# Kernel tuning notes

Hardware: AMD Instinct MI355X
Metric: run time of the kernel (lower is better)

## Reference

```python
import jax, jax.numpy as jnp
import numpy as np

N_NODES = 50000
N_EDGES = 600000
N_ELEMENTS = 100
N_RBF = 50
D = 128
CUTOFF = 5.0


def setup_inputs() -> dict:
    key = jax.random.key(0)
    ks = jax.random.split(key, 10)
    node_type = jax.random.randint(ks[0], (N_NODES,), 0, N_ELEMENTS)
    x_nodes = jax.random.normal(ks[1], (N_NODES, D), dtype=jnp.float32)
    src = jax.random.randint(ks[2], (N_EDGES,), 0, N_NODES)
    dst = jax.random.randint(ks[3], (N_EDGES,), 0, N_NODES)
    rbf_edges = jax.random.normal(ks[4], (N_EDGES, N_RBF), dtype=jnp.float32)
    dist = jax.random.uniform(ks[5], (N_EDGES,), dtype=jnp.float32) * (CUTOFF * 1.2)
    emb = jax.random.normal(ks[6], (N_ELEMENTS, D), dtype=jnp.float32) * 0.1
    W_e = jax.random.normal(ks[7], (D, N_RBF), dtype=jnp.float32) * (1.0 / np.sqrt(N_RBF))
    b_e = jnp.zeros((D,), dtype=jnp.float32)
    W_c = jax.random.normal(ks[8], (D, 2 * D), dtype=jnp.float32) * (1.0 / np.sqrt(2 * D))
    b_c = jnp.zeros((D,), dtype=jnp.float32)
    return {"node_type": node_type, "x_nodes": x_nodes, "src": src, "dst": dst,
            "rbf_edges": rbf_edges, "dist": dist, "emb": emb,
            "W_e": W_e, "b_e": b_e, "W_c": W_c, "b_c": b_c}


def cosine_cutoff(dist, cutoff):
    # 0.5*(cos(pi*d/cutoff)+1), zeroed beyond cutoff
    w = 0.5 * (jnp.cos(dist * (jnp.pi / cutoff)) + 1.0)
    return w * (dist < cutoff).astype(dist.dtype)


def reference(node_type, x_nodes, src, dst, rbf_edges, dist, emb, W_e, b_e, W_c, b_c):
    # node embedding from atom type: [N, D]
    x_neighbors = emb[node_type]
    # edge projection weighted by cutoff: [E, D]
    x_edges = (rbf_edges @ W_e.T + b_e) * cosine_cutoff(dist, CUTOFF)[:, None]
    # gather source node embedding, multiply by edge embedding, scatter-sum to dst
    msg = x_neighbors[src] * x_edges  # [E, D]
    x_integrated = jax.ops.segment_sum(msg, dst, num_segments=N_NODES)  # [N, D]
    # concat + combine linear: [N, D]
    x_combine = jnp.concatenate([x_nodes, x_integrated], axis=-1)
    return x_combine @ W_c.T + b_c
```

## Files before the change

### kernel.cpp

```cpp
#include <hip/hip_runtime.h>
#include <hip/hip_bf16.h>

constexpr int NN   = 50000;
constexpr int NE   = 600000;
constexpr int NRBF = 50;
constexpr int DIM  = 128;
constexpr float CUT = 5.0f;
constexpr float PI_F = 3.14159265358979323846f;

constexpr int CAP = 64;

constexpr size_t OFF_DEG  = 0;
constexpr size_t OFF_OVFC = OFF_DEG  + (size_t)NN * 4;
constexpr size_t OFF_EID  = 200960;
constexpr size_t OFF_OVF  = OFF_EID  + (size_t)NN * CAP * 4;
constexpr size_t OFF_MSG  = OFF_OVF  + (size_t)NE * 4;
constexpr size_t OFF_XI   = OFF_MSG  + (size_t)NE * DIM * 2;

typedef __attribute__((ext_vector_type(4))) float f32x4;
typedef __attribute__((ext_vector_type(8))) short short8;

__device__ __forceinline__ float bf2f(unsigned short u) {
    return __uint_as_float(((unsigned int)u) << 16);
}

__global__ __launch_bounds__(256)
void build_buckets(const int* __restrict__ dst, const float* __restrict__ dist,
                   int* __restrict__ deg, int* __restrict__ eid,
                   int* __restrict__ ovf, int* __restrict__ ovf_cnt)
{
    const int e = blockIdx.x * 256 + threadIdx.x;
    if (e >= NE) return;
    if (dist[e] < CUT) {
        const int n = dst[e];
        const int pos = atomicAdd(&deg[n], 1);
        if (pos < CAP) eid[n * CAP + pos] = e;
        else           ovf[atomicAdd(ovf_cnt, 1)] = e;
    }
}

__global__ __launch_bounds__(256)
void edge_msg_kernel(const float* __restrict__ rbf, const float* __restrict__ dist,
                     const int* __restrict__ src, const int* __restrict__ node_type,
                     const float* __restrict__ emb, const float* __restrict__ W_e,
                     const float* __restrict__ b_e, __hip_bfloat16* __restrict__ msg)
{
    __shared__ unsigned short As[64][72];
    __shared__ unsigned short Bs[128][72];
    __shared__ float cc_s[64];
    __shared__ int   embrow_s[64];

    const int t  = threadIdx.x;
    const int e0 = blockIdx.x * 64;

    {
        const int r = t >> 2, c = t & 3;
        const float2* row = (const float2*)(rbf + (size_t)(e0 + r) * NRBF);
        #pragma unroll
        for (int s = 0; s < 7; ++s) {
            const int idx = c + 4 * s;
            if (idx < 25) {
                const float2 v = row[idx];
                As[r][2 * idx]     = __bfloat16_as_ushort(__float2bfloat16(v.x));
                As[r][2 * idx + 1] = __bfloat16_as_ushort(__float2bfloat16(v.y));
            }
        }
        *(ushort2*)&As[r][50 + 2 * c] = make_ushort2(0, 0);
        *(ushort2*)&As[r][58 + 2 * c] = make_ushort2(0, 0);
    }
    {
        const int r = t >> 1, c = t & 1;
        const float2* row = (const float2*)(W_e + (size_t)r * NRBF);
        #pragma unroll
        for (int s = 0; s < 13; ++s) {
            const int idx = c + 2 * s;
            if (idx < 25) {
                const float2 v = row[idx];
                Bs[r][2 * idx]     = __bfloat16_as_ushort(__float2bfloat16(v.x));
                Bs[r][2 * idx + 1] = __bfloat16_as_ushort(__float2bfloat16(v.y));
            }
        }
        #pragma unroll
        for (int q = 0; q < 4; ++q)
            *(ushort2*)&Bs[r][50 + 4 * q + 2 * c] = make_ushort2(0, 0);
    }
    if (t < 64) {
        const int e = e0 + t;
        const float dd = dist[e];
        const float w  = 0.5f * (__cosf(dd * (PI_F / CUT)) + 1.0f);
        cc_s[t]     = (dd < CUT) ? w : 0.0f;
        embrow_s[t] = node_type[src[e]];
    }
    __syncthreads();

    const int wv = t >> 6, l = t & 63;
    f32x4 acc[8] = {};
    #pragma unroll
    for (int s = 0; s < 2; ++s) {
        const int ko = s * 32 + (l >> 4) * 8;
        const short8 af = *(const short8*)&As[wv * 16 + (l & 15)][ko];
        #pragma unroll
        for (int nt = 0; nt < 8; ++nt) {
            const short8 bf = *(const short8*)&Bs[nt * 16 + (l & 15)][ko];
            acc[nt] = __builtin_amdgcn_mfma_f32_16x16x32_bf16(af, bf, acc[nt], 0, 0, 0);
        }
    }

    const int col = l & 15;
    const int rq  = (l >> 4) * 4;
    float be[8];
    #pragma unroll
    for (int nt = 0; nt < 8; ++nt) be[nt] = b_e[nt * 16 + col];

    #pragma unroll
    for (int r = 0; r < 4; ++r) {
        const int el = wv * 16 + rq + r;
        const float cc = cc_s[el];
        if (cc != 0.0f) {
            const int erow = embrow_s[el];
            __hip_bfloat16* mrow = msg + (size_t)(e0 + el) * DIM;
            #pragma unroll
            for (int nt = 0; nt < 8; ++nt) {
                const int dim = nt * 16 + col;
                const float v = (acc[nt][r] + be[nt]) * cc * emb[(size_t)erow * DIM + dim];
                mrow[dim] = __float2bfloat16(v);
            }
        }
    }
}

__global__ __launch_bounds__(256)
void gather_sum(const __hip_bfloat16* __restrict__ msg, const int* __restrict__ deg,
                const int* __restrict__ eid, const int* __restrict__ ovf,
                const int* __restrict__ ovf_cnt, const int* __restrict__ dst,
                __hip_bfloat16* __restrict__ xi)
{
    const int t    = threadIdx.x;
    const int lane = t & 63;
    const int n    = blockIdx.x * 4 + (t >> 6);
    if (n >= NN) return;

    const int dn   = deg[n];
    const int degn = dn < CAP ? dn : CAP;
    int eidv = 0;
    if (lane < degn) eidv = eid[n * CAP + lane];

    float ax = 0.0f, ay = 0.0f;
    int j = 0;
    for (; j + 4 <= degn; j += 4) {
        const int ea = __shfl(eidv, j);
        const int eb = __shfl(eidv, j + 1);
        const int ec = __shfl(eidv, j + 2);
        const int ed = __shfl(eidv, j + 3);
        const ushort2 va = ((const ushort2*)(msg + (size_t)ea * DIM))[lane];
        const ushort2 vb = ((const ushort2*)(msg + (size_t)eb * DIM))[lane];
        const ushort2 vc = ((const ushort2*)(msg + (size_t)ec * DIM))[lane];
        const ushort2 vd = ((const ushort2*)(msg + (size_t)ed * DIM))[lane];
        ax += bf2f(va.x) + bf2f(vb.x) + bf2f(vc.x) + bf2f(vd.x);
        ay += bf2f(va.y) + bf2f(vb.y) + bf2f(vc.y) + bf2f(vd.y);
    }
    for (; j < degn; ++j) {
        const int e = __shfl(eidv, j);
        const ushort2 v = ((const ushort2*)(msg + (size_t)e * DIM))[lane];
        ax += bf2f(v.x);
        ay += bf2f(v.y);
    }
    const int ocnt = ovf_cnt[0];
    for (j = 0; j < ocnt; ++j) {
        const int e = ovf[j];
        if (dst[e] == n) {
            const ushort2 v = ((const ushort2*)(msg + (size_t)e * DIM))[lane];
            ax += bf2f(v.x);
            ay += bf2f(v.y);
        }
    }

    ushort2 st;
    st.x = __bfloat16_as_ushort(__float2bfloat16(ax));
    st.y = __bfloat16_as_ushort(__float2bfloat16(ay));
    ((ushort2*)(xi + (size_t)n * DIM))[lane] = st;
}

__global__ __launch_bounds__(256)
void combine_mfma(const float* __restrict__ x_nodes, const __hip_bfloat16* __restrict__ xi,
                  const float* __restrict__ W_c, const float* __restrict__ b_c,
                  float* __restrict__ out)
{
    __shared__ unsigned short As[64][72];
    __shared__ unsigned short Bs[128][72];

    const int t  = threadIdx.x;
    const int wv = t >> 6;
    const int l  = t & 63;
    const int n0 = blockIdx.x * 64;

    f32x4 acc[8] = {};

    for (int kc = 0; kc < 4; ++kc) {
        const int kb = kc * 64;
        if (kc) __syncthreads();
        {
            const int r  = t >> 2;
            const int c0 = (t & 3) * 16;
            const int n  = n0 + r;
            if (kc < 2) {
                float4 v[4];
                if (n < NN) {
                    const float4* p = (const float4*)(x_nodes + (size_t)n * DIM + kb + c0);
                    v[0] = p[0]; v[1] = p[1]; v[2] = p[2]; v[3] = p[3];
                } else {
                    v[0] = v[1] = v[2] = v[3] = make_float4(0.f, 0.f, 0.f, 0.f);
                }
                unsigned short* dp = &As[r][c0];
                #pragma unroll
                for (int q = 0; q < 4; ++q) {
                    dp[q * 4 + 0] = __bfloat16_as_ushort(__float2bfloat16(v[q].x));
                    dp[q * 4 + 1] = __bfloat16_as_ushort(__float2bfloat16(v[q].y));
                    dp[q * 4 + 2] = __bfloat16_as_ushort(__float2bfloat16(v[q].z));
                    dp[q * 4 + 3] = __bfloat16_as_ushort(__float2bfloat16(v[q].w));
                }
            } else {
                int4 v0 = make_int4(0, 0, 0, 0), v1 = make_int4(0, 0, 0, 0);
                if (n < NN) {
                    const int4* p = (const int4*)(xi + (size_t)n * DIM + (kb - DIM) + c0);
                    v0 = p[0];
                    v1 = p[1];
                }
                *(int4*)&As[r][c0]     = v0;
                *(int4*)&As[r][c0 + 8] = v1;
            }
        }
        {
            const int dch = t >> 1;
            const int c0  = (t & 1) * 32;
            const float4* p = (const float4*)(W_c + (size_t)dch * (2 * DIM) + kb + c0);
            unsigned short* dp = &Bs[dch][c0];
            #pragma unroll
            for (int q = 0; q < 8; ++q) {
                const float4 v = p[q];
                dp[q * 4 + 0] = __bfloat16_as_ushort(__float2bfloat16(v.x));
                dp[q * 4 + 1] = __bfloat16_as_ushort(__float2bfloat16(v.y));
                dp[q * 4 + 2] = __bfloat16_as_ushort(__float2bfloat16(v.z));
                dp[q * 4 + 3] = __bfloat16_as_ushort(__float2bfloat16(v.w));
            }
        }
        __syncthreads();
        #pragma unroll
        for (int s = 0; s < 2; ++s) {
            const int ko = s * 32 + (l >> 4) * 8;
            const short8 af = *(const short8*)&As[wv * 16 + (l & 15)][ko];
            #pragma unroll
            for (int nt = 0; nt < 8; ++nt) {
                const short8 bf = *(const short8*)&Bs[nt * 16 + (l & 15)][ko];
                acc[nt] = __builtin_amdgcn_mfma_f32_16x16x32_bf16(af, bf, acc[nt], 0, 0, 0);
            }
        }
    }

    const int col = l & 15;
    const int rq  = (l >> 4) * 4;
    #pragma unroll
    for (int nt = 0; nt < 8; ++nt) {
        const int dim = nt * 16 + col;
        const float bc = b_c[dim];
        #pragma unroll
        for (int r = 0; r < 4; ++r) {
            const int node = n0 + wv * 16 + rq + r;
            if (node < NN)
                out[(size_t)node * DIM + dim] = acc[nt][r] + bc;
        }
    }
}

extern "C" void kernel_launch(void* const* d_in, const int* in_sizes, int n_in,
                              void* d_out, int out_size, void* d_ws, size_t ws_size,
                              hipStream_t stream)
{
    const int*   node_type = (const int*)  d_in[0];
    const float* x_nodes   = (const float*)d_in[1];
    const int*   src       = (const int*)  d_in[2];
    const int*   dst       = (const int*)  d_in[3];
    const float* rbf       = (const float*)d_in[4];
    const float* dist      = (const float*)d_in[5];
    const float* emb       = (const float*)d_in[6];
    const float* W_e       = (const float*)d_in[7];
    const float* b_e       = (const float*)d_in[8];
    const float* W_c       = (const float*)d_in[9];
    const float* b_c       = (const float*)d_in[10];
    float* out = (float*)d_out;

    char* ws = (char*)d_ws;
    int*            deg     = (int*)(ws + OFF_DEG);
    int*            ovf_cnt = (int*)(ws + OFF_OVFC);
    int*            eid     = (int*)(ws + OFF_EID);
    int*            ovf     = (int*)(ws + OFF_OVF);
    __hip_bfloat16* msg     = (__hip_bfloat16*)(ws + OFF_MSG);
    __hip_bfloat16* xi      = (__hip_bfloat16*)(ws + OFF_XI);

    hipMemsetAsync(deg, 0, (NN + 1) * sizeof(int), stream);

    build_buckets<<<(NE + 255) / 256, 256, 0, stream>>>(dst, dist, deg, eid, ovf, ovf_cnt);

    edge_msg_kernel<<<NE / 64, 256, 0, stream>>>(rbf, dist, src, node_type, emb,
                                                 W_e, b_e, msg);

    gather_sum<<<(NN + 3) / 4, 256, 0, stream>>>(msg, deg, eid, ovf, ovf_cnt, dst, xi);

    combine_mfma<<<(NN + 63) / 64, 256, 0, stream>>>(x_nodes, xi, W_c, b_c, out);
}
```

Baseline: 369.3 us.

## Store edge messages in permuted packed layout, process four edge tiles per block

New measurement: 357.6 us. -3.2%, faster.

```diff
diff --git a/kernel.cpp b/kernel.cpp
--- a/kernel.cpp
+++ b/kernel.cpp
@@ -17,11 +17,15 @@
 constexpr size_t OFF_MSG  = OFF_OVF  + (size_t)NE * 4;
 constexpr size_t OFF_XI   = OFF_MSG  + (size_t)NE * DIM * 2;
 
+
 typedef __attribute__((ext_vector_type(4))) float f32x4;
 typedef __attribute__((ext_vector_type(8))) short short8;
 
 __device__ __forceinline__ float bf2f(unsigned short u) {
     return __uint_as_float(((unsigned int)u) << 16);
+}
+__device__ __forceinline__ unsigned short f2bf(float f) {
+    return __bfloat16_as_ushort(__float2bfloat16(f));
 }
 
 __global__ __launch_bounds__(256)
@@ -51,23 +55,10 @@
     __shared__ int   embrow_s[64];
 
     const int t  = threadIdx.x;
-    const int e0 = blockIdx.x * 64;
-
-    {
-        const int r = t >> 2, c = t & 3;
-        const float2* row = (const float2*)(rbf + (size_t)(e0 + r) * NRBF);
-        #pragma unroll
-        for (int s = 0; s < 7; ++s) {
-            const int idx = c + 4 * s;
-            if (idx < 25) {
-                const float2 v = row[idx];
-                As[r][2 * idx]     = __bfloat16_as_ushort(__float2bfloat16(v.x));
-                As[r][2 * idx + 1] = __bfloat16_as_ushort(__float2bfloat16(v.y));
-            }
-        }
-        *(ushort2*)&As[r][50 + 2 * c] = make_ushort2(0, 0);
-        *(ushort2*)&As[r][58 + 2 * c] = make_ushort2(0, 0);
-    }
+    const int wv = t >> 6, l = t & 63;
+    const int col = l & 15;
+    const int rq  = (l >> 4) * 4;
+
     {
         const int r = t >> 1, c = t & 1;
         const float2* row = (const float2*)(W_e + (size_t)r * NRBF);
@@ -76,54 +67,75 @@
             const int idx = c + 2 * s;
             if (idx < 25) {
                 const float2 v = row[idx];
-                Bs[r][2 * idx]     = __bfloat16_as_ushort(__float2bfloat16(v.x));
-                Bs[r][2 * idx + 1] = __bfloat16_as_ushort(__float2bfloat16(v.y));
+                *(ushort2*)&Bs[r][2 * idx] = make_ushort2(f2bf(v.x), f2bf(v.y));
             }
         }
         #pragma unroll
         for (int q = 0; q < 4; ++q)
             *(ushort2*)&Bs[r][50 + 4 * q + 2 * c] = make_ushort2(0, 0);
     }
-    if (t < 64) {
-        const int e = e0 + t;
-        const float dd = dist[e];
-        const float w  = 0.5f * (__cosf(dd * (PI_F / CUT)) + 1.0f);
-        cc_s[t]     = (dd < CUT) ? w : 0.0f;
-        embrow_s[t] = node_type[src[e]];
-    }
-    __syncthreads();
-
-    const int wv = t >> 6, l = t & 63;
-    f32x4 acc[8] = {};
-    #pragma unroll
-    for (int s = 0; s < 2; ++s) {
-        const int ko = s * 32 + (l >> 4) * 8;
-        const short8 af = *(const short8*)&As[wv * 16 + (l & 15)][ko];
-        #pragma unroll
-        for (int nt = 0; nt < 8; ++nt) {
-            const short8 bf = *(const short8*)&Bs[nt * 16 + (l & 15)][ko];
-            acc[nt] = __builtin_amdgcn_mfma_f32_16x16x32_bf16(af, bf, acc[nt], 0, 0, 0);
-        }
-    }
-
-    const int col = l & 15;
-    const int rq  = (l >> 4) * 4;
+
     float be[8];
     #pragma unroll
     for (int nt = 0; nt < 8; ++nt) be[nt] = b_e[nt * 16 + col];
 
-    #pragma unroll
-    for (int r = 0; r < 4; ++r) {
-        const int el = wv * 16 + rq + r;
-        const float cc = cc_s[el];
-        if (cc != 0.0f) {
-            const int erow = embrow_s[el];
-            __hip_bfloat16* mrow = msg + (size_t)(e0 + el) * DIM;
+    for (int tile = 0; tile < 4; ++tile) {
+        const int e0 = (blockIdx.x * 4 + tile) * 64;
+        if (e0 >= NE) break;
+        if (tile) __syncthreads();
+
+        {
+            const int r = t >> 2, c = t & 3;
+            const float2* row = (const float2*)(rbf + (size_t)(e0 + r) * NRBF);
+            #pragma unroll
+            for (int s = 0; s < 7; ++s) {
+                const int idx = c + 4 * s;
+                if (idx < 25) {
+                    const float2 v = row[idx];
+                    *(ushort2*)&As[r][2 * idx] = make_ushort2(f2bf(v.x), f2bf(v.y));
+                }
+            }
+            *(ushort2*)&As[r][50 + 2 * c] = make_ushort2(0, 0);
+            *(ushort2*)&As[r][58 + 2 * c] = make_ushort2(0, 0);
+        }
+        if (t < 64) {
+            const int e = e0 + t;
+            const float dd = dist[e];
+            const float w  = 0.5f * (__cosf(dd * (PI_F / CUT)) + 1.0f);
+            cc_s[t]     = (dd < CUT) ? w : 0.0f;
+            embrow_s[t] = node_type[src[e]];
+        }
+        __syncthreads();
+
+        f32x4 acc[8] = {};
+        #pragma unroll
+        for (int s = 0; s < 2; ++s) {
+            const int ko = s * 32 + (l >> 4) * 8;
+            const short8 af = *(const short8*)&As[wv * 16 + (l & 15)][ko];
             #pragma unroll
             for (int nt = 0; nt < 8; ++nt) {
-                const int dim = nt * 16 + col;
-                const float v = (acc[nt][r] + be[nt]) * cc * emb[(size_t)erow * DIM + dim];
-                mrow[dim] = __float2bfloat16(v);
+                const short8 bf = *(const short8*)&Bs[nt * 16 + (l & 15)][ko];
+                acc[nt] = __builtin_amdgcn_mfma_f32_16x16x32_bf16(af, bf, acc[nt], 0, 0, 0);
+            }
+        }
+
+        #pragma unroll
+        for (int r = 0; r < 4; ++r) {
+            const int el = wv * 16 + rq + r;
+            const float cc = cc_s[el];
+            if (cc != 0.0f) {
+                const int erow = embrow_s[el];
+                unsigned int w[4];
+                #pragma unroll
+                for (int q = 0; q < 4; ++q) {
+                    const float v0 = (acc[2 * q][r]     + be[2 * q])     * cc *
+                                     emb[(size_t)erow * DIM + (2 * q) * 16 + col];
+                    const float v1 = (acc[2 * q + 1][r] + be[2 * q + 1]) * cc *
+                                     emb[(size_t)erow * DIM + (2 * q + 1) * 16 + col];
+                    w[q] = (unsigned int)f2bf(v0) | ((unsigned int)f2bf(v1) << 16);
+                }
+                int4* dp = (int4*)(msg + (size_t)(e0 + el) * DIM + 8 * col);
+                *dp = make_int4((int)w[0], (int)w[1], (int)w[2], (int)w[3]);
             }
         }
     }
@@ -175,10 +187,18 @@
         }
     }
 
-    ushort2 st;
-    st.x = __bfloat16_as_ushort(__float2bfloat16(ax));
-    st.y = __bfloat16_as_ushort(__float2bfloat16(ay));
-    ((ushort2*)(xi + (size_t)n * DIM))[lane] = st;
+    const int d0  = 2 * lane;
+    const int p_a = ((d0 & 15) << 3) + (d0 >> 4);
+    const int s0  = p_a >> 1;
+    const int cmp = p_a & 1;
+    const float A1 = __shfl(ax, s0);
+    const float B1 = __shfl(ay, s0);
+    const float A2 = __shfl(ax, s0 + 4);
+    const float B2 = __shfl(ay, s0 + 4);
+    const float va = cmp ? B1 : A1;
+    const float vb = cmp ? B2 : A2;
+
+    ((ushort2*)(xi + (size_t)n * DIM))[lane] = make_ushort2(f2bf(va), f2bf(vb));
 }
 
 __global__ __launch_bounds__(256)
@@ -214,10 +234,8 @@
                 unsigned short* dp = &As[r][c0];
                 #pragma unroll
                 for (int q = 0; q < 4; ++q) {
-                    dp[q * 4 + 0] = __bfloat16_as_ushort(__float2bfloat16(v[q].x));
-                    dp[q * 4 + 1] = __bfloat16_as_ushort(__float2bfloat16(v[q].y));
-                    dp[q * 4 + 2] = __bfloat16_as_ushort(__float2bfloat16(v[q].z));
-                    dp[q * 4 + 3] = __bfloat16_as_ushort(__float2bfloat16(v[q].w));
+                    *(ushort2*)&dp[q * 4]     = make_ushort2(f2bf(v[q].x), f2bf(v[q].y));
+                    *(ushort2*)&dp[q * 4 + 2] = make_ushort2(f2bf(v[q].z), f2bf(v[q].w));
                 }
             } else {
                 int4 v0 = make_int4(0, 0, 0, 0), v1 = make_int4(0, 0, 0, 0);
@@ -238,10 +256,8 @@
             #pragma unroll
             for (int q = 0; q < 8; ++q) {
                 const float4 v = p[q];
-                dp[q * 4 + 0] = __bfloat16_as_ushort(__float2bfloat16(v.x));
-                dp[q * 4 + 1] = __bfloat16_as_ushort(__float2bfloat16(v.y));
-                dp[q * 4 + 2] = __bfloat16_as_ushort(__float2bfloat16(v.z));
-                dp[q * 4 + 3] = __bfloat16_as_ushort(__float2bfloat16(v.w));
+                *(ushort2*)&dp[q * 4]     = make_ushort2(f2bf(v.x), f2bf(v.y));
+                *(ushort2*)&dp[q * 4 + 2] = make_ushort2(f2bf(v.z), f2bf(v.w));
             }
         }
         __syncthreads();
@@ -301,8 +317,8 @@
 
     build_buckets<<<(NE + 255) / 256, 256, 0, stream>>>(dst, dist, deg, eid, ovf, ovf_cnt);
 
-    edge_msg_kernel<<<NE / 64, 256, 0, stream>>>(rbf, dist, src, node_type, emb,
-                                                 W_e, b_e, msg);
+    edge_msg_kernel<<<(NE / 64 + 3) / 4, 256, 0, stream>>>(rbf, dist, src, node_type, emb,
+                                                           W_e, b_e, msg);
 
     gather_sum<<<(NN + 3) / 4, 256, 0, stream>>>(msg, deg, eid, ovf, ovf_cnt, dst, xi);
 
```
